# Kernel tuning notes

Measured on AMD Instinct MI355X. Metric: run time of the kernel, lower is better.

## Reference

```python
import jax, jax.numpy as jnp
import numpy as np

NEG_SLOPE = 0.2


def gat_conv(x, W, att_s, att_d, bias, src, dst, heads, out_c, concat):
    n = x.shape[0]
    h = (x @ W).reshape(n, heads, out_c)                      # [N,H,C]
    a_s = (h * att_s).sum(-1)                                 # [N,H]
    a_d = (h * att_d).sum(-1)                                 # [N,H]
    logits = jax.nn.leaky_relu(a_s[src] + a_d[dst], NEG_SLOPE)  # [E,H]
    # segment softmax over incoming edges of each dst node (per head)
    m = jax.ops.segment_max(logits, dst, num_segments=n)
    e = jnp.exp(logits - m[dst])
    denom = jax.ops.segment_sum(e, dst, num_segments=n)
    alpha = e / denom[dst]                                    # [E,H]
    msg = h[src] * alpha[:, :, None]                          # [E,H,C]
    out = jax.ops.segment_sum(msg, dst, num_segments=n)       # [N,H,C]
    out = out.reshape(n, heads * out_c) if concat else out.mean(axis=1)
    return out + bias


def setup_inputs() -> dict:
    key = jax.random.key(0)
    ks = jax.random.split(key, 9)
    N, IN, OUT, E = 100000, 256, 40, 1600000
    return {
        "x": jax.random.normal(ks[0], (N, IN), jnp.float32),
        "edge_index": jax.random.randint(ks[1], (2, E), 0, N, jnp.int32),
        "W1": jax.random.normal(ks[2], (IN, 64), jnp.float32) * (1.0 / np.sqrt(IN)),
        "att_src1": jax.random.normal(ks[3], (8, 8), jnp.float32) * 0.1,
        "att_dst1": jax.random.normal(ks[4], (8, 8), jnp.float32) * 0.1,
        "b1": jnp.zeros((64,), jnp.float32),
        "W2": jax.random.normal(ks[5], (64, OUT), jnp.float32) * (1.0 / 8.0),
        "att_src2": jax.random.normal(ks[6], (1, OUT), jnp.float32) * 0.1,
        "att_dst2": jax.random.normal(ks[7], (1, OUT), jnp.float32) * 0.1,
        "b2": jnp.zeros((OUT,), jnp.float32),
    }


def reference(x, edge_index, W1, att_src1, att_dst1, b1, W2, att_src2, att_dst2, b2):
    n = x.shape[0]
    loop = jnp.arange(n, dtype=edge_index.dtype)
    src = jnp.concatenate([edge_index[0], loop])  # self-loops (PyG default)
    dst = jnp.concatenate([edge_index[1], loop])
    h = gat_conv(x, W1, att_src1, att_dst1, b1, src, dst, heads=8, out_c=8, concat=True)
    h = jax.nn.relu(h)
    out = gat_conv(h, W2, att_src2, att_dst2, b2, src, dst, heads=1, out_c=W2.shape[1], concat=True)
    return jax.nn.log_softmax(out, axis=1)
```

## Files before the change

kernel.cpp:

```cpp
#include <hip/hip_runtime.h>


#define L_IN   256
#define L_C1   64
#define L_H1   8
#define L_OUT  40
#define BCAP   5120

typedef __attribute__((ext_vector_type(8))) short short8;
typedef __attribute__((ext_vector_type(4))) float f32x4;

__device__ __forceinline__ float leaky(float x){ return fmaxf(x, 0.2f*x); }
__device__ __forceinline__ unsigned f2bf(float f){
  unsigned u = __float_as_uint(f);
  return (u + 0x7fffu + ((u >> 16) & 1u)) >> 16;
}
__device__ __forceinline__ float bflo(unsigned u){ return __uint_as_float(u << 16); }
__device__ __forceinline__ float bfhi(unsigned u){ return __uint_as_float(u & 0xffff0000u); }

__global__ __launch_bounds__(256) void prep_w1(const float* __restrict__ W1,
                                               ushort* __restrict__ wt,
                                               int* __restrict__ gcur, int NB){
  const int t = threadIdx.x;
  if (blockIdx.x == 4){
    for (int i = t; i < NB; i += 256) gcur[i] = 0;
    return;
  }
  __shared__ float ws[64][65];
  const int kb = blockIdx.x;
  #pragma unroll
  for (int i = 0; i < 16; ++i){
    int idx = t + i*256;
    ws[idx >> 6][idx & 63] = W1[(size_t)(kb*64 + (idx >> 6))*64 + (idx & 63)];
  }
  __syncthreads();
  int c  = t >> 2;
  int j0 = (t & 3) * 16;
  ushort tmp[16];
  #pragma unroll
  for (int j = 0; j < 16; ++j) tmp[j] = (ushort)f2bf(ws[j0 + j][c]);
  uint4* dst = (uint4*)(wt + (size_t)c*256 + kb*64 + j0);
  dst[0] = *(uint4*)&tmp[0];
  dst[1] = *(uint4*)&tmp[8];
}

__global__ __launch_bounds__(256) void bin_scatter(const int* __restrict__ esrc,
    const int* __restrict__ edst, int* __restrict__ gcur,
    unsigned* __restrict__ binned, int E, int NB){
  __shared__ int hist[512], rbase[512], cur[512];
  const int t  = threadIdx.x;
  const int e0 = blockIdx.x * 4096;
  hist[t] = 0; hist[t+256] = 0; cur[t] = 0; cur[t+256] = 0;
  __syncthreads();
  int sv[16], dv[16];
  const bool full = (e0 + 4096 <= E);
  if (full){
    #pragma unroll
    for (int j = 0; j < 4; ++j){
      int p4 = (e0 >> 2) + j*256 + t;
      int4 s4 = ((const int4*)esrc)[p4];
      int4 d4 = ((const int4*)edst)[p4];
      sv[4*j+0]=s4.x; sv[4*j+1]=s4.y; sv[4*j+2]=s4.z; sv[4*j+3]=s4.w;
      dv[4*j+0]=d4.x; dv[4*j+1]=d4.y; dv[4*j+2]=d4.z; dv[4*j+3]=d4.w;
      atomicAdd(&hist[d4.x >> 8], 1); atomicAdd(&hist[d4.y >> 8], 1);
      atomicAdd(&hist[d4.z >> 8], 1); atomicAdd(&hist[d4.w >> 8], 1);
    }
  } else {
    #pragma unroll
    for (int j = 0; j < 16; ++j){
      int idx = e0 + j*256 + t;
      if (idx < E){
        sv[j] = esrc[idx]; dv[j] = edst[idx];
        atomicAdd(&hist[dv[j] >> 8], 1);
      } else dv[j] = -1;
    }
  }
  __syncthreads();
  if (hist[t])                   rbase[t]     = atomicAdd(&gcur[t],     hist[t]);
  if (t+256 < NB && hist[t+256]) rbase[t+256] = atomicAdd(&gcur[t+256], hist[t+256]);
  __syncthreads();
  #pragma unroll
  for (int j = 0; j < 16; ++j){
    if (dv[j] >= 0){
      int b = dv[j] >> 8;
      int off = rbase[b] + atomicAdd(&cur[b], 1);
      if (off < BCAP)
        binned[(size_t)b*BCAP + off] =
          (unsigned)sv[j] | ((unsigned)(dv[j] & 255) << 17);
    }
  }
}

__global__ __launch_bounds__(256) void gemm1_kernel(
    const float* __restrict__ x, const ushort* __restrict__ wt,
    const float* __restrict__ atts, const float* __restrict__ attd,
    ushort* __restrict__ h1b, float* __restrict__ as1, float* __restrict__ ad1,
    int n, int ntiles, int npb)
{
  __shared__ ushort ws[64][264];
  __shared__ ushort hs[64][72];
  const int t  = threadIdx.x;
  const int wv = t >> 6;
  const int ln = t & 63;
  const int fr = ln & 15;
  const int fq = ln >> 4;

  #pragma unroll
  for (int i = 0; i < 8; ++i){
    int idx = t + i*256;
    int row = idx >> 5, c8 = idx & 31;
    *(uint4*)&ws[row][c8*8] = *(const uint4*)(wt + (size_t)row*256 + c8*8);
  }
  __syncthreads();

  for (int tile = blockIdx.x; tile < ntiles; tile += npb){
    const int rb = tile * 64;
    const int ar = rb + wv*16 + fr;
    const bool rv = ar < n;
    const float* xr = x + (size_t)(rv ? ar : 0) * L_IN;

    f32x4 acc[4];
    #pragma unroll
    for (int cb = 0; cb < 4; ++cb) acc[cb] = (f32x4){0.f,0.f,0.f,0.f};

    #pragma unroll
    for (int kk = 0; kk < 8; ++kk){
      const int k0 = kk*32 + fq*8;
      float4 a0 = make_float4(0.f,0.f,0.f,0.f), a1 = a0;
      if (rv){
        a0 = *(const float4*)(xr + k0);
        a1 = *(const float4*)(xr + k0 + 4);
      }
      uint4 au;
      au.x = f2bf(a0.x) | (f2bf(a0.y) << 16);
      au.y = f2bf(a0.z) | (f2bf(a0.w) << 16);
      au.z = f2bf(a1.x) | (f2bf(a1.y) << 16);
      au.w = f2bf(a1.z) | (f2bf(a1.w) << 16);
      short8 a = *(short8*)&au;
      #pragma unroll
      for (int cb = 0; cb < 4; ++cb){
        short8 b = *(const short8*)&ws[cb*16 + fr][k0];
        acc[cb] = __builtin_amdgcn_mfma_f32_16x16x32_bf16(a, b, acc[cb], 0, 0, 0);
      }
    }

    #pragma unroll
    for (int cb = 0; cb < 4; ++cb)
      #pragma unroll
      for (int r = 0; r < 4; ++r)
        hs[wv*16 + fq*4 + r][cb*16 + fr] = (ushort)f2bf(acc[cb][r]);

    #pragma unroll
    for (int i = 0; i < 2; ++i){
      int task = ln + i*64;
      int lrow = task >> 3;
      int sub  = task & 7;
      int row  = rb + wv*16 + lrow;
      if (row < n){
        uint4 u = *(const uint4*)&hs[wv*16 + lrow][sub*8];
        *(uint4*)(h1b + (size_t)row*L_C1 + sub*8) = u;
        float v0=bflo(u.x), v1=bfhi(u.x), v2=bflo(u.y), v3=bfhi(u.y);
        float v4=bflo(u.z), v5=bfhi(u.z), v6=bflo(u.w), v7=bfhi(u.w);
        const float* sa = atts + sub*8;
        const float* da = attd + sub*8;
        float ds = v0*sa[0]+v1*sa[1]+v2*sa[2]+v3*sa[3]+v4*sa[4]+v5*sa[5]+v6*sa[6]+v7*sa[7];
        float dd = v0*da[0]+v1*da[1]+v2*da[2]+v3*da[3]+v4*da[4]+v5*da[5]+v6*da[6]+v7*da[7];
        as1[(size_t)row*L_H1 + sub] = ds;
        ad1[(size_t)row*L_H1 + sub] = dd;
      }
    }
  }
}

__global__ __launch_bounds__(512) void bucket_csr(const unsigned* __restrict__ binned,
    const int* __restrict__ gcur, int2* __restrict__ nodeptr, int* __restrict__ csr,
    int N){
  __shared__ unsigned ebuf[BCAP];
  __shared__ int cnt[256], pref[256], cur[256];
  const int t = threadIdx.x;
  const int b = blockIdx.x;
  int ne = gcur[b]; if (ne > BCAP) ne = BCAP;
  const int base = b * BCAP;
  if (t < 256){ cnt[t] = 0; cur[t] = 0; }
  __syncthreads();
  for (int i = t; i < ne; i += 512){
    unsigned e = binned[base + i];
    ebuf[i] = e;
    atomicAdd(&cnt[(e >> 17) & 255u], 1);
  }
  __syncthreads();
  if (t < 256) pref[t] = cnt[t];
  __syncthreads();
  for (int off = 1; off < 256; off <<= 1){
    int a = 0;
    if (t < 256 && t >= off) a = pref[t-off];
    __syncthreads();
    if (t < 256) pref[t] += a;
    __syncthreads();
  }
  int excl = 0;
  if (t < 256) excl = pref[t] - cnt[t];
  __syncthreads();
  if (t < 256){
    pref[t] = excl;
    int d = (b << 8) + t;
    if (d < N) nodeptr[d] = make_int2(base + excl, cnt[t]);
  }
  __syncthreads();
  for (int i = t; i < ne; i += 512){
    unsigned e = ebuf[i];
    int ln = (int)((e >> 17) & 255u);
    int pos = base + pref[ln] + atomicAdd(&cur[ln], 1);
    csr[pos] = (int)(e & 0x1FFFFu);
  }
}

__global__ __launch_bounds__(256) void agg1_kernel(
    const int2* __restrict__ nodeptr, const int* __restrict__ csr,
    const ushort* __restrict__ h1b, const float* __restrict__ as1,
    const float* __restrict__ ad1, const float* __restrict__ b1,
    ushort* __restrict__ hrb, int n)
{
  int wid  = (blockIdx.x*blockDim.x + threadIdx.x) >> 6;
  int lane = threadIdx.x & 63;
  if (wid >= n) return;
  int2 np  = nodeptr[wid];
  int beg  = np.x;
  int degt = np.y + 1;

  const int h  = lane & 7;
  const int eg = lane >> 3;
  const int cp = lane & 31;
  const int ep = lane >> 5;
  const int hc = cp >> 2;

  float adn = ad1[(size_t)wid*L_H1 + h];
  float ax = 0.f, ay = 0.f, sp = 0.f;

  #define A1_GRP_W(g, SRCV, WV)                                            \
    { int i_ = (g)*8 + eg;                                                 \
      SRCV = (i_ < degt-1) ? csr[beg + i_] : wid;                          \
      float l_ = (i_ < degt) ? leaky(as1[(size_t)SRCV*L_H1 + h] + adn)     \
                             : -1e30f;                                     \
      WV = __expf(l_); sp += WV; }
  #define A1_GRP_G(SRCV, WV)                                               \
    _Pragma("unroll")                                                      \
    for (int e0 = 0; e0 < 8; e0 += 2){                                     \
      int e_  = e0 + ep;                                                   \
      float we_ = __shfl(WV,   e_*8 + hc);                                 \
      int   se_ = __shfl(SRCV, e_*8);                                      \
      unsigned u_ = *(const unsigned*)(h1b + (size_t)se_*L_C1 + cp*2);     \
      ax += we_ * bflo(u_);                                                \
      ay += we_ * bfhi(u_);                                                \
    }

  if (degt <= 16){
    int s0, s1; float w0, w1;
    A1_GRP_W(0, s0, w0) A1_GRP_W(1, s1, w1)
    A1_GRP_G(s0, w0) A1_GRP_G(s1, w1)
  } else if (degt <= 24){
    int s0, s1, s2; float w0, w1, w2;
    A1_GRP_W(0, s0, w0) A1_GRP_W(1, s1, w1) A1_GRP_W(2, s2, w2)
    A1_GRP_G(s0, w0) A1_GRP_G(s1, w1) A1_GRP_G(s2, w2)
  } else {
    const int ngrp = (degt + 7) >> 3;
    for (int g = 0; g < ngrp; ++g){
      int sg; float wg;
      A1_GRP_W(g, sg, wg)
      A1_GRP_G(sg, wg)
    }
  }
  #undef A1_GRP_W
  #undef A1_GRP_G

  #pragma unroll
  for (int off = 8; off < 64; off <<= 1) sp += __shfl_xor(sp, off);
  float rinv = 1.0f / __shfl(sp, hc);
  ax += __shfl_xor(ax, 32);
  ay += __shfl_xor(ay, 32);
  if (lane < 32){
    float2 bv = *(const float2*)&b1[cp*2];
    float r0 = fmaxf(ax*rinv + bv.x, 0.f);
    float r1 = fmaxf(ay*rinv + bv.y, 0.f);
    *(unsigned*)(hrb + (size_t)wid*L_C1 + cp*2) = f2bf(r0) | (f2bf(r1) << 16);
  }
}

__global__ __launch_bounds__(256) void gemm2_kernel(
    const ushort* __restrict__ hrb, const float* __restrict__ W2,
    const float* __restrict__ atts2, const float* __restrict__ attd2,
    ushort* __restrict__ h2b, float* __restrict__ as2, float* __restrict__ ad2, int n)
{
  __shared__ float w2s[64*40];
  const int t = threadIdx.x;
  for (int i = t; i < 64*40; i += 256) w2s[i] = W2[i];
  __syncthreads();
  int row = blockIdx.x*256 + t;
  if (row >= n) return;

  uint4 rv[8];
  #pragma unroll
  for (int q = 0; q < 8; ++q)
    rv[q] = *(const uint4*)(hrb + (size_t)row*L_C1 + q*8);

  f32x4 acc4[10];
  #pragma unroll
  for (int j = 0; j < 10; ++j) acc4[j] = (f32x4){0.f,0.f,0.f,0.f};

  #pragma unroll
  for (int q = 0; q < 8; ++q){
    unsigned uu[4] = {rv[q].x, rv[q].y, rv[q].z, rv[q].w};
    #pragma unroll
    for (int d = 0; d < 4; ++d){
      int k = q*8 + d*2;
      float v0 = bflo(uu[d]), v1 = bfhi(uu[d]);
      const f32x4* w0 = (const f32x4*)&w2s[k*40];
      const f32x4* w1 = (const f32x4*)&w2s[(k+1)*40];
      #pragma unroll
      for (int j = 0; j < 10; ++j) acc4[j] += v0*w0[j] + v1*w1[j];
    }
  }

  float acc[40];
  #pragma unroll
  for (int j = 0; j < 10; ++j){
    acc[4*j+0]=acc4[j][0]; acc[4*j+1]=acc4[j][1];
    acc[4*j+2]=acc4[j][2]; acc[4*j+3]=acc4[j][3];
  }
  float ps = 0.f, pd = 0.f;
  #pragma unroll
  for (int j = 0; j < 40; ++j){ ps += acc[j]*atts2[j]; pd += acc[j]*attd2[j]; }
  unsigned pk[20];
  #pragma unroll
  for (int q = 0; q < 20; ++q) pk[q] = f2bf(acc[2*q]) | (f2bf(acc[2*q+1]) << 16);
  uint4* dst = (uint4*)(h2b + (size_t)row*L_OUT);
  #pragma unroll
  for (int q = 0; q < 5; ++q) dst[q] = make_uint4(pk[4*q],pk[4*q+1],pk[4*q+2],pk[4*q+3]);
  as2[row] = ps;
  ad2[row] = pd;
}

__global__ __launch_bounds__(256) void agg2_kernel(
    const int2* __restrict__ nodeptr, const int* __restrict__ csr,
    const ushort* __restrict__ h2b, const float* __restrict__ as2,
    const float* __restrict__ ad2, const float* __restrict__ b2,
    float* __restrict__ out, int n)
{
  int wid  = (blockIdx.x*blockDim.x + threadIdx.x) >> 6;
  int lane = threadIdx.x & 63;
  if (wid >= n) return;
  int2 np  = nodeptr[wid];
  int beg  = np.x;
  int degt = np.y + 1;

  const int eidx = (lane < 60) ? (lane / 20) : 0;
  const int cq   = (lane < 60) ? (lane % 20) : 0;

  float adn = ad2[wid];
  float ax = 0.f, ay = 0.f, sp = 0.f;

  #define A2_STEP(e_, SRCV, WV, CNT)                                       \
    { int ee_ = (e_);                                                      \
      int es_ = (ee_ < 64) ? ee_ : 63;                                     \
      float we_ = __shfl(WV,   es_);                                       \
      int   se_ = __shfl(SRCV, es_);                                       \
      we_ = (ee_ < (CNT)) ? we_ : 0.f;                                     \
      unsigned u_ = *(const unsigned*)(h2b + (size_t)se_*L_OUT + cq*2);    \
      ax += we_ * bflo(u_);                                                \
      ay += we_ * bfhi(u_); }

  if (degt <= 64){
    int i = lane;
    int src = (i < degt-1) ? csr[beg + i] : wid;
    float l = (i < degt) ? leaky(as2[src] + adn) : -1e30f;
    float w = __expf(l);
    sp = w;
    if (degt <= 18){
      #pragma unroll
      for (int j = 0; j < 2; ++j){
        A2_STEP(j*9 + 0*3 + eidx, src, w, degt)
        A2_STEP(j*9 + 1*3 + eidx, src, w, degt)
        A2_STEP(j*9 + 2*3 + eidx, src, w, degt)
      }
    } else if (degt <= 27){
      #pragma unroll
      for (int j = 0; j < 3; ++j){
        A2_STEP(j*9 + 0*3 + eidx, src, w, degt)
        A2_STEP(j*9 + 1*3 + eidx, src, w, degt)
        A2_STEP(j*9 + 2*3 + eidx, src, w, degt)
      }
    } else if (degt <= 36){
      #pragma unroll
      for (int j = 0; j < 4; ++j){
        A2_STEP(j*9 + 0*3 + eidx, src, w, degt)
        A2_STEP(j*9 + 1*3 + eidx, src, w, degt)
        A2_STEP(j*9 + 2*3 + eidx, src, w, degt)
      }
    } else {
      for (int e0 = 0; e0 < degt; e0 += 9){
        A2_STEP(e0 + 0*3 + eidx, src, w, degt)
        A2_STEP(e0 + 1*3 + eidx, src, w, degt)
        A2_STEP(e0 + 2*3 + eidx, src, w, degt)
      }
    }
  } else {
    const int ngrp = (degt + 63) >> 6;
    for (int g = 0; g < ngrp; ++g){
      int i = g*64 + lane;
      int src = (i < degt-1) ? csr[beg + i] : wid;
      float l = (i < degt) ? leaky(as2[src] + adn) : -1e30f;
      float w = __expf(l);
      sp += w;
      int cnt = degt - g*64; if (cnt > 64) cnt = 64;
      for (int e0 = 0; e0 < cnt; e0 += 9){
        A2_STEP(e0 + 0*3 + eidx, src, w, cnt)
        A2_STEP(e0 + 1*3 + eidx, src, w, cnt)
        A2_STEP(e0 + 2*3 + eidx, src, w, cnt)
      }
    }
  }
  #undef A2_STEP

  #pragma unroll
  for (int off = 1; off < 64; off <<= 1) sp += __shfl_xor(sp, off);
  float rinv = 1.0f / sp;

  float ax0 = __shfl(ax, cq), ax1 = __shfl(ax, cq+20), ax2 = __shfl(ax, cq+40);
  float ay0 = __shfl(ay, cq), ay1 = __shfl(ay, cq+20), ay2 = __shfl(ay, cq+40);
  float axs = (ax0 + ax1) + ax2;
  float ays = (ay0 + ay1) + ay2;

  bool act = (lane < 20);
  float o0 = axs*rinv + b2[cq*2];
  float o1 = ays*rinv + b2[cq*2+1];
  float mx = act ? fmaxf(o0, o1) : -1e30f;
  #pragma unroll
  for (int off = 1; off < 32; off <<= 1) mx = fmaxf(mx, __shfl_xor(mx, off));
  float ex = act ? (__expf(o0 - mx) + __expf(o1 - mx)) : 0.f;
  #pragma unroll
  for (int off = 1; off < 32; off <<= 1) ex += __shfl_xor(ex, off);
  float lse = mx + __logf(ex);
  if (act){
    float2 r = make_float2(o0 - lse, o1 - lse);
    *(float2*)(out + (size_t)wid*L_OUT + cq*2) = r;
  }
}

extern "C" void kernel_launch(void* const* d_in, const int* in_sizes, int n_in,
                              void* d_out, int out_size, void* d_ws, size_t ws_size,
                              hipStream_t stream)
{
  const float* x    = (const float*)d_in[0];
  const int*   ei   = (const int*)  d_in[1];
  const float* W1   = (const float*)d_in[2];
  const float* as1w = (const float*)d_in[3];
  const float* ad1w = (const float*)d_in[4];
  const float* b1   = (const float*)d_in[5];
  const float* W2   = (const float*)d_in[6];
  const float* as2w = (const float*)d_in[7];
  const float* ad2w = (const float*)d_in[8];
  const float* b2   = (const float*)d_in[9];

  const int N = in_sizes[0] / L_IN;
  const int E = in_sizes[1] / 2;
  const int NB = (N + 255) >> 8;
  const int NSC = (E + 4095) / 4096;
  const int NT1 = (N + 63) / 64;
  const int NPB = (NT1 < 768) ? NT1 : 768;
  const int* esrc = ei;
  const int* edst = ei + E;
  float* out = (float*)d_out;

  char* w = (char*)d_ws;
  auto alloc = [&](size_t bytes)->char*{
    char* p = w; w += (bytes + 255) & ~size_t(255); return p;
  };
  ushort* h1b  = (ushort*)alloc((size_t)N*L_C1*2);
  float*  as1  = (float*) alloc((size_t)N*L_H1*4);
  float*  ad1  = (float*) alloc((size_t)N*L_H1*4);
  size_t union_sz = (size_t)N*L_C1*2 + (size_t)N*L_OUT*2;
  if (union_sz < (size_t)NB*BCAP*4) union_sz = (size_t)NB*BCAP*4;
  char*  ub    = alloc(union_sz);
  ushort* hrb  = (ushort*)ub;
  ushort* h2b  = (ushort*)(ub + (size_t)N*L_C1*2);
  unsigned* binned = (unsigned*)ub;
  float*  as2  = (float*) alloc((size_t)N*4);
  float*  ad2  = (float*) alloc((size_t)N*4);
  ushort* wt   = (ushort*)alloc((size_t)64*256*2);
  int2*  nodeptr=(int2*)  alloc((size_t)N*8);
  int*   csr   = (int*)   alloc((size_t)NB*BCAP*4);
  int*   gcur  = (int*)   alloc((size_t)NB*4);

  prep_w1     <<<5,          256, 0, stream>>>(W1, wt, gcur, NB);
  bin_scatter <<<NSC,        256, 0, stream>>>(esrc, edst, gcur, binned, E, NB);
  gemm1_kernel<<<NPB,        256, 0, stream>>>(x, wt, as1w, ad1w, h1b, as1, ad1,
                                               N, NT1, NPB);
  bucket_csr  <<<NB,         512, 0, stream>>>(binned, gcur, nodeptr, csr, N);
  agg1_kernel <<<(N+3)/4,    256, 0, stream>>>(nodeptr, csr, h1b, as1, ad1, b1, hrb, N);
  gemm2_kernel<<<(N+255)/256,256, 0, stream>>>(hrb, W2, as2w, ad2w, h2b, as2, ad2, N);
  agg2_kernel <<<(N+3)/4,    256, 0, stream>>>(nodeptr, csr, h2b, as2, ad2, b2, out, N);
}
```

Before: 183.8 us.

## Merge CSR bucket build into GEMM1 launch and widen agg1 gathers to 8 bytes

The bucket-to-CSR conversion now runs as the first NB blocks of a combined kernel, and the remaining blocks do the layer-1 GEMM. This removes one launch and lets the two independent stages run at the same time on the GPU. The bucket part drops from 512 to 256 threads per block, and the combined kernel sizes its shared memory for the larger of the two uses. Separately, agg1 now has each lane gather 4 bf16 channels (uint2) instead of 2, processing 4 edges per step with 16 lanes each, which adds an extra cross-lane reduction at the end.

```diff
diff --git a/kernel.cpp b/kernel.cpp
--- a/kernel.cpp
+++ b/kernel.cpp
@@ -91,15 +91,59 @@
   }
 }
 
-__global__ __launch_bounds__(256) void gemm1_kernel(
+__global__ __launch_bounds__(256) void csr_gemm1(
+    const unsigned* __restrict__ binned, const int* __restrict__ gcur,
+    int2* __restrict__ nodeptr, int* __restrict__ csr, int NBK,
     const float* __restrict__ x, const ushort* __restrict__ wt,
     const float* __restrict__ atts, const float* __restrict__ attd,
     ushort* __restrict__ h1b, float* __restrict__ as1, float* __restrict__ ad1,
     int n, int ntiles, int npb)
 {
-  __shared__ ushort ws[64][264];
-  __shared__ ushort hs[64][72];
-  const int t  = threadIdx.x;
+  __shared__ __align__(16) char smem[43008];
+  const int t   = threadIdx.x;
+  const int bid = blockIdx.x;
+
+  if (bid < NBK){
+    unsigned* ebuf = (unsigned*)smem;
+    int* cnt  = (int*)(smem + BCAP*4);
+    int* pref = cnt + 256;
+    int* cur  = pref + 256;
+    const int b = bid;
+    int ne = gcur[b]; if (ne > BCAP) ne = BCAP;
+    const int base = b * BCAP;
+    cnt[t] = 0; cur[t] = 0;
+    __syncthreads();
+    for (int i = t; i < ne; i += 256){
+      unsigned e = binned[base + i];
+      ebuf[i] = e;
+      atomicAdd(&cnt[(e >> 17) & 255u], 1);
+    }
+    __syncthreads();
+    pref[t] = cnt[t];
+    __syncthreads();
+    for (int off = 1; off < 256; off <<= 1){
+      int a = (t >= off) ? pref[t-off] : 0;
+      __syncthreads();
+      pref[t] += a;
+      __syncthreads();
+    }
+    int excl = pref[t] - cnt[t];
+    __syncthreads();
+    pref[t] = excl;
+    int d = (b << 8) + t;
+    if (d < n) nodeptr[d] = make_int2(base + excl, cnt[t]);
+    __syncthreads();
+    for (int i = t; i < ne; i += 256){
+      unsigned e = ebuf[i];
+      int ln = (int)((e >> 17) & 255u);
+      int pos = base + pref[ln] + atomicAdd(&cur[ln], 1);
+      csr[pos] = (int)(e & 0x1FFFFu);
+    }
+    return;
+  }
+
+  ushort (*ws)[264] = (ushort(*)[264])(smem);
+  ushort (*hs)[72]  = (ushort(*)[72]) (smem + 33792);
   const int wv = t >> 6;
   const int ln = t & 63;
   const int fr = ln & 15;
@@ -113,7 +157,7 @@
   }
   __syncthreads();
 
-  for (int tile = blockIdx.x; tile < ntiles; tile += npb){
+  for (int tile = bid - NBK; tile < ntiles; tile += npb){
     const int rb = tile * 64;
     const int ar = rb + wv*16 + fr;
     const bool rv = ar < n;
@@ -172,49 +216,6 @@
   }
 }
 
-__global__ __launch_bounds__(512) void bucket_csr(const unsigned* __restrict__ binned,
-    const int* __restrict__ gcur, int2* __restrict__ nodeptr, int* __restrict__ csr,
-    int N){
-  __shared__ unsigned ebuf[BCAP];
-  __shared__ int cnt[256], pref[256], cur[256];
-  const int t = threadIdx.x;
-  const int b = blockIdx.x;
-  int ne = gcur[b]; if (ne > BCAP) ne = BCAP;
-  const int base = b * BCAP;
-  if (t < 256){ cnt[t] = 0; cur[t] = 0; }
-  __syncthreads();
-  for (int i = t; i < ne; i += 512){
-    unsigned e = binned[base + i];
-    ebuf[i] = e;
-    atomicAdd(&cnt[(e >> 17) & 255u], 1);
-  }
-  __syncthreads();
-  if (t < 256) pref[t] = cnt[t];
-  __syncthreads();
-  for (int off = 1; off < 256; off <<= 1){
-    int a = 0;
-    if (t < 256 && t >= off) a = pref[t-off];
-    __syncthreads();
-    if (t < 256) pref[t] += a;
-    __syncthreads();
-  }
-  int excl = 0;
-  if (t < 256) excl = pref[t] - cnt[t];
-  __syncthreads();
-  if (t < 256){
-    pref[t] = excl;
-    int d = (b << 8) + t;
-    if (d < N) nodeptr[d] = make_int2(base + excl, cnt[t]);
-  }
-  __syncthreads();
-  for (int i = t; i < ne; i += 512){
-    unsigned e = ebuf[i];
-    int ln = (int)((e >> 17) & 255u);
-    int pos = base + pref[ln] + atomicAdd(&cur[ln], 1);
-    csr[pos] = (int)(e & 0x1FFFFu);
-  }
-}
-
 __global__ __launch_bounds__(256) void agg1_kernel(
     const int2* __restrict__ nodeptr, const int* __restrict__ csr,
     const ushort* __restrict__ h1b, const float* __restrict__ as1,
@@ -230,12 +231,12 @@
 
   const int h  = lane & 7;
   const int eg = lane >> 3;
-  const int cp = lane & 31;
-  const int ep = lane >> 5;
-  const int hc = cp >> 2;
+  const int cq = lane & 15;
+  const int eq = lane >> 4;
+  const int hw = cq >> 1;
 
   float adn = ad1[(size_t)wid*L_H1 + h];
-  float ax = 0.f, ay = 0.f, sp = 0.f;
+  float a0 = 0.f, a1 = 0.f, a2 = 0.f, a3 = 0.f, sp = 0.f;
 
   #define A1_GRP_W(g, SRCV, WV)                                            \
     { int i_ = (g)*8 + eg;                                                 \
@@ -245,13 +246,15 @@
       WV = __expf(l_); sp += WV; }
   #define A1_GRP_G(SRCV, WV)                                               \
     _Pragma("unroll")                                                      \
-    for (int e0 = 0; e0 < 8; e0 += 2){                                     \
-      int e_  = e0 + ep;                                                   \
-      float we_ = __shfl(WV,   e_*8 + hc);                                 \
+    for (int e0 = 0; e0 < 8; e0 += 4){                                     \
+      int e_  = e0 + eq;                                                   \
+      float we_ = __shfl(WV,   e_*8 + hw);                                 \
       int   se_ = __shfl(SRCV, e_*8);                                      \
-      unsigned u_ = *(const unsigned*)(h1b + (size_t)se_*L_C1 + cp*2);     \
-      ax += we_ * bflo(u_);                                                \
-      ay += we_ * bfhi(u_);                                                \
+      uint2 u_ = *(const uint2*)(h1b + (size_t)se_*L_C1 + cq*4);           \
+      a0 += we_ * bflo(u_.x);                                              \
+      a1 += we_ * bfhi(u_.x);                                              \
+      a2 += we_ * bflo(u_.y);                                              \
+      a3 += we_ * bfhi(u_.y);                                              \
     }
 
   if (degt <= 16){
@@ -275,14 +278,21 @@
 
   #pragma unroll
   for (int off = 8; off < 64; off <<= 1) sp += __shfl_xor(sp, off);
-  float rinv = 1.0f / __shfl(sp, hc);
-  ax += __shfl_xor(ax, 32);
-  ay += __shfl_xor(ay, 32);
-  if (lane < 32){
-    float2 bv = *(const float2*)&b1[cp*2];
-    float r0 = fmaxf(ax*rinv + bv.x, 0.f);
-    float r1 = fmaxf(ay*rinv + bv.y, 0.f);
-    *(unsigned*)(hrb + (size_t)wid*L_C1 + cp*2) = f2bf(r0) | (f2bf(r1) << 16);
+  float rinv = 1.0f / __shfl(sp, hw);
+  a0 += __shfl_xor(a0, 16); a0 += __shfl_xor(a0, 32);
+  a1 += __shfl_xor(a1, 16); a1 += __shfl_xor(a1, 32);
+  a2 += __shfl_xor(a2, 16); a2 += __shfl_xor(a2, 32);
+  a3 += __shfl_xor(a3, 16); a3 += __shfl_xor(a3, 32);
+  if (lane < 16){
+    float4 bv = *(const float4*)&b1[cq*4];
+    float r0 = fmaxf(a0*rinv + bv.x, 0.f);
+    float r1 = fmaxf(a1*rinv + bv.y, 0.f);
+    float r2 = fmaxf(a2*rinv + bv.z, 0.f);
+    float r3 = fmaxf(a3*rinv + bv.w, 0.f);
+    uint2 o;
+    o.x = f2bf(r0) | (f2bf(r1) << 16);
+    o.y = f2bf(r2) | (f2bf(r3) << 16);
+    *(uint2*)(hrb + (size_t)wid*L_C1 + cq*4) = o;
   }
 }
 
@@ -493,9 +503,9 @@
 
   prep_w1     <<<5,          256, 0, stream>>>(W1, wt, gcur, NB);
   bin_scatter <<<NSC,        256, 0, stream>>>(esrc, edst, gcur, binned, E, NB);
-  gemm1_kernel<<<NPB,        256, 0, stream>>>(x, wt, as1w, ad1w, h1b, as1, ad1,
+  csr_gemm1   <<<NB + NPB,   256, 0, stream>>>(binned, gcur, nodeptr, csr, NB,
+                                               x, wt, as1w, ad1w, h1b, as1, ad1,
                                                N, NT1, NPB);
-  bucket_csr  <<<NB,         512, 0, stream>>>(binned, gcur, nodeptr, csr, N);
   agg1_kernel <<<(N+3)/4,    256, 0, stream>>>(nodeptr, csr, h1b, as1, ad1, b1, hrb, N);
   gemm2_kernel<<<(N+255)/256,256, 0, stream>>>(hrb, W2, as2w, ad2w, h2b, as2, ad2, N);
   agg2_kernel <<<(N+3)/4,    256, 0, stream>>>(nodeptr, csr, h2b, as2, ad2, b2, out, N);
```

After: 175.5 us. 4.5% less time.
